# Kernel optimization log

Measured on AMD Instinct MI355X. Metric: run time of the kernel, lower is better.

## Reference

```python
import jax, jax.numpy as jnp
import numpy as np

DN = ('NCDHW', 'OIDHW', 'NCDHW')

def conv3d(x, w, b=None):
    y = jax.lax.conv_general_dilated(x, w, (1, 1, 1), 'SAME', dimension_numbers=DN)
    if b is not None:
        y = y + b[None, :, None, None, None]
    return y

def adaptive_conv(x, w):
    # x: [N,C,D,H,W], w: [N,27,D,H,W] (L1-normalized over channel dim)
    D, H, W = x.shape[2], x.shape[3], x.shape[4]
    p = jnp.pad(x, ((0, 0), (0, 0), (1, 1), (1, 1), (1, 1)))
    out = jnp.zeros_like(x)
    for i in range(3):
        for j in range(3):
            for k in range(3):
                t = i * 9 + j * 3 + k
                out = out + p[:, :, i:i + D, j:j + H, k:k + W] * w[:, t:t + 1]
    return out

def l1_normalize(w):
    # torch F.normalize(dim=1, p=1): denom clamped to 1e-12
    denom = jnp.maximum(jnp.sum(jnp.abs(w), axis=1, keepdims=True), 1e-12)
    return w / denom

def adaptive_block(x, w1, b1, w2, weights_src=None):
    src = x if weights_src is None else weights_src
    h = jax.nn.relu(conv3d(src, w1, b1))
    w = l1_normalize(conv3d(h, w2))  # [N,27,D,H,W]
    for _ in range(3):
        x = adaptive_conv(x, w)
    return x

def setup_inputs() -> dict:
    key = jax.random.key(0)
    ks = jax.random.split(key, 16)
    s = 0.05
    inp = {
        'x': jax.random.normal(ks[0], (1, 8, 128, 128, 128), dtype=jnp.float32),
        'ac1_w1': jax.random.normal(ks[1], (8, 8, 3, 3, 3), dtype=jnp.float32) * s,
        'ac1_b1': jnp.zeros((8,), dtype=jnp.float32),
        'ac1_w2': jax.random.normal(ks[2], (27, 8, 3, 3, 3), dtype=jnp.float32) * s,
        'ac2_w1': jax.random.normal(ks[3], (8, 8, 3, 3, 3), dtype=jnp.float32) * s,
        'ac2_b1': jnp.zeros((8,), dtype=jnp.float32),
        'ac2_w2': jax.random.normal(ks[4], (27, 8, 3, 3, 3), dtype=jnp.float32) * s,
        'ac3_w1': jax.random.normal(ks[5], (8, 8, 3, 3, 3), dtype=jnp.float32) * s,
        'ac3_b1': jnp.zeros((8,), dtype=jnp.float32),
        'ac3_w2': jax.random.normal(ks[6], (27, 8, 3, 3, 3), dtype=jnp.float32) * s,
        'mid_w': jax.random.normal(ks[7], (8, 8, 3, 3, 3), dtype=jnp.float32) * s,
        'mid_b': jnp.zeros((8,), dtype=jnp.float32),
        'out_w': jax.random.normal(ks[8], (1, 8, 3, 3, 3), dtype=jnp.float32) * s,
        'out_b': jnp.zeros((1,), dtype=jnp.float32),
    }
    return inp

def reference(x, ac1_w1, ac1_b1, ac1_w2, ac2_w1, ac2_b1, ac2_w2,
              ac3_w1, ac3_b1, ac3_w2, mid_w, mid_b, out_w, out_b):
    mid = adaptive_block(x, ac1_w1, ac1_b1, ac1_w2)
    mid = conv3d(mid, mid_w, mid_b)
    mid = adaptive_block(mid, ac2_w1, ac2_b1, ac2_w2)
    final = conv3d(mid, out_w, out_b)  # [N,1,D,H,W]
    final = adaptive_block(final, ac3_w1, ac3_b1, ac3_w2, weights_src=mid)
    return jnp.tanh(final)
```

## Files before the change

### kernel.cpp

```cpp
#include <hip/hip_runtime.h>
#include <math.h>

#define DSZ 128
#define VOX (DSZ*DSZ*DSZ)
#define PD  130

typedef _Float16 half8 __attribute__((ext_vector_type(8)));
typedef _Float16 half4 __attribute__((ext_vector_type(4)));
typedef _Float16 half2v __attribute__((ext_vector_type(2)));
typedef float float4v __attribute__((ext_vector_type(4)));


template<int CH>
__global__ __launch_bounds__(256) void zero_halo(_Float16* __restrict__ P)
{
    const int t = blockIdx.x * 256 + threadIdx.x;
    if (t >= PD * PD) return;
    const int zp = t / PD;
    const int yp = t - zp * PD;
    _Float16* row = P + (size_t)t * PD * CH;
    if (zp == 0 || zp == PD - 1 || yp == 0 || yp == PD - 1) {
        if (CH == 8) {
            half8 zz = {};
            for (int x = 0; x < PD; ++x) *(half8*)&row[x * 8] = zz;
        } else {
            for (int x = 0; x < PD; ++x) row[x] = (_Float16)0.0f;
        }
    } else {
        if (CH == 8) {
            half8 zz = {};
            *(half8*)&row[0] = zz;
            *(half8*)&row[(PD - 1) * 8] = zz;
        } else {
            row[0] = (_Float16)0.0f;
            row[PD - 1] = (_Float16)0.0f;
        }
    }
}

__global__ __launch_bounds__(256) void preformat(const float* __restrict__ w1a, const float* __restrict__ w1b,
                                                 const float* __restrict__ w1c, const float* __restrict__ outw,
                                                 const float* __restrict__ midw,
                                                 const float* __restrict__ w2a, const float* __restrict__ w2b,
                                                 const float* __restrict__ w2c, _Float16* __restrict__ WF)
{
    const int bid = blockIdx.x, tid = threadIdx.x;
    const float* src;
    _Float16* dst;
    int nelem, sz;
    if (bid < 3)       { src = bid == 0 ? w1a : bid == 1 ? w1b : w1c; dst = WF + bid * 3712; nelem = 8 * 216; sz = 16 * 29; }
    else if (bid == 3) { src = outw; dst = WF + 3 * 3712; nelem = 216;     sz = 16 * 29; }
    else if (bid == 4) { src = midw; dst = WF + 4 * 3712; nelem = 8 * 216; sz = 16 * 29; }
    else               { src = bid == 5 ? w2a : bid == 6 ? w2b : w2c; dst = WF + 5 * 3712 + (bid - 5) * 7424; nelem = 27 * 216; sz = 32 * 29; }
    for (int i = tid; i < sz; i += 256) ((half8*)dst)[i] = half8{};
    __syncthreads();
    for (int i = tid; i < nelem; i += 256) {
        const int oc = i / 216;
        const int rem = i - oc * 216;
        const int ic = rem / 27;
        const int tap = rem - ic * 27;
        dst[(oc * 29 + tap) * 8 + ic] = (_Float16)src[i];
    }
}

__global__ __launch_bounds__(256) void cast_hp(const float* __restrict__ in,
                                               _Float16* __restrict__ hp)
{
    const int idx = blockIdx.x * 256 + threadIdx.x;
    const int w = idx & 127;
    const int h = (idx >> 7) & 127;
    const int d = idx >> 14;
    half8 v;
    #pragma unroll
    for (int ic = 0; ic < 8; ++ic) v[ic] = (_Float16)in[(size_t)ic * VOX + idx];
    const int slot = ((d + 1) * PD + (h + 1)) * PD + (w + 1);
    *(half8*)&hp[(size_t)slot * 8] = v;
}

template<bool RELU>
__global__ __launch_bounds__(256) void conv8x8_mfma(const _Float16* __restrict__ DP,
                                                    const _Float16* __restrict__ WF,
                                                    const float* __restrict__ bias,
                                                    _Float16* __restrict__ HO)
{
    __shared__ _Float16 Wr[16 * 29 * 8];
    const int tid = threadIdx.x;
    for (int i = tid; i < 16 * 29; i += 256) ((half8*)Wr)[i] = ((const half8*)WF)[i];
    __syncthreads();

    const int b = ((blockIdx.x & 7) << 10) | (blockIdx.x >> 3);
    const int h0 = (b & 63) << 1;
    const int d  = b >> 6;
    const int lane = tid & 63;
    const int wv   = tid >> 6;
    const int col  = lane & 15;
    const int q    = lane >> 4;

    half8 af[7];
    #pragma unroll
    for (int c = 0; c < 7; ++c)
        af[c] = *(const half8*)&Wr[(col * 29 + (c * 4 + q)) * 8];

    const int base0 = ((d + 1) * PD + (h0 + 1)) * PD + 1 + wv * 32 + col;
    const _Float16* p[7];
    #pragma unroll
    for (int c = 0; c < 7; ++c) {
        const int tap = min(c * 4 + q, 26);
        const int dz = tap / 9, r9 = tap - dz * 9;
        const int dy = r9 / 3,  dx = r9 - dy * 3;
        p[c] = DP + (size_t)(base0 + ((dz - 1) * PD + (dy - 1)) * PD + (dx - 1)) * 8;
    }

    #pragma unroll
    for (int r = 0; r < 2; ++r) {
        #pragma unroll
        for (int t2 = 0; t2 < 2; ++t2) {
            float4v acc = {0.0f, 0.0f, 0.0f, 0.0f};
            #pragma unroll
            for (int c = 0; c < 7; ++c) {
                const half8 bv = *(const half8*)(p[c] + (r * PD + t2 * 16) * 8);
                acc = __builtin_amdgcn_mfma_f32_16x16x32_f16(af[c], bv, acc, 0, 0, 0);
            }
            if (q < 2) {
                const float4v bl = ((const float4v*)bias)[q];
                half4 hv;
                #pragma unroll
                for (int rr = 0; rr < 4; ++rr) {
                    float v = acc[rr] + bl[rr];
                    if (RELU) v = fmaxf(v, 0.0f);
                    hv[rr] = (_Float16)v;
                }
                *(half4*)&HO[(size_t)(base0 + r * PD + t2 * 16) * 8 + q * 4] = hv;
            }
        }
    }
}

__global__ __launch_bounds__(256) void conv8x1_mfma(const _Float16* __restrict__ DP,
                                                    const _Float16* __restrict__ WF,
                                                    const float* __restrict__ bias,
                                                    _Float16* __restrict__ F)
{
    __shared__ _Float16 Wr[16 * 29 * 8];
    const int tid = threadIdx.x;
    for (int i = tid; i < 16 * 29; i += 256) ((half8*)Wr)[i] = ((const half8*)WF)[i];
    __syncthreads();

    const int b = ((blockIdx.x & 7) << 10) | (blockIdx.x >> 3);
    const int h0 = (b & 63) << 1;
    const int d  = b >> 6;
    const int lane = tid & 63;
    const int wv   = tid >> 6;
    const int col  = lane & 15;
    const int q    = lane >> 4;

    half8 af[7];
    #pragma unroll
    for (int c = 0; c < 7; ++c)
        af[c] = *(const half8*)&Wr[(col * 29 + (c * 4 + q)) * 8];

    const int base0 = ((d + 1) * PD + (h0 + 1)) * PD + 1 + wv * 32 + col;
    const _Float16* p[7];
    #pragma unroll
    for (int c = 0; c < 7; ++c) {
        const int tap = min(c * 4 + q, 26);
        const int dz = tap / 9, r9 = tap - dz * 9;
        const int dy = r9 / 3,  dx = r9 - dy * 3;
        p[c] = DP + (size_t)(base0 + ((dz - 1) * PD + (dy - 1)) * PD + (dx - 1)) * 8;
    }

    const float b0 = bias[0];
    #pragma unroll
    for (int r = 0; r < 2; ++r) {
        #pragma unroll
        for (int t2 = 0; t2 < 2; ++t2) {
            float4v acc = {0.0f, 0.0f, 0.0f, 0.0f};
            #pragma unroll
            for (int c = 0; c < 7; ++c) {
                const half8 bv = *(const half8*)(p[c] + (r * PD + t2 * 16) * 8);
                acc = __builtin_amdgcn_mfma_f32_16x16x32_f16(af[c], bv, acc, 0, 0, 0);
            }
            if (q == 0)
                F[base0 + r * PD + t2 * 16] = (_Float16)(acc[0] + b0);
        }
    }
}

__global__ __launch_bounds__(256) void conv8x27n_mfma(const _Float16* __restrict__ HP,
                                                      const _Float16* __restrict__ WF,
                                                      _Float16* __restrict__ WB)
{
    __shared__ _Float16 Wr[32 * 29 * 8];
    const int tid = threadIdx.x;
    for (int i = tid; i < 32 * 29; i += 256) ((half8*)Wr)[i] = ((const half8*)WF)[i];
    __syncthreads();

    const int b = ((blockIdx.x & 7) << 10) | (blockIdx.x >> 3);
    const int h0 = (b & 63) << 1;
    const int d  = b >> 6;
    const int lane = tid & 63;
    const int wv   = tid >> 6;
    const int col  = lane & 15;
    const int q    = lane >> 4;

    half8 af[2][7];
    #pragma unroll
    for (int t = 0; t < 2; ++t)
        #pragma unroll
        for (int c = 0; c < 7; ++c)
            af[t][c] = *(const half8*)&Wr[((t * 16 + col) * 29 + (c * 4 + q)) * 8];

    const int base0 = ((d + 1) * PD + (h0 + 1)) * PD + 1 + wv * 32 + col;
    const _Float16* p[7];
    #pragma unroll
    for (int c = 0; c < 7; ++c) {
        const int tap = min(c * 4 + q, 26);
        const int dz = tap / 9, r9 = tap - dz * 9;
        const int dy = r9 / 3,  dx = r9 - dy * 3;
        p[c] = HP + (size_t)(base0 + ((dz - 1) * PD + (dy - 1)) * PD + (dx - 1)) * 8;
    }

    #pragma unroll
    for (int r = 0; r < 2; ++r) {
        #pragma unroll
        for (int t2 = 0; t2 < 2; ++t2) {
            float4v acc0 = {0.0f, 0.0f, 0.0f, 0.0f};
            float4v acc1 = {0.0f, 0.0f, 0.0f, 0.0f};
            #pragma unroll
            for (int c = 0; c < 7; ++c) {
                const half8 bv = *(const half8*)(p[c] + (r * PD + t2 * 16) * 8);
                acc0 = __builtin_amdgcn_mfma_f32_16x16x32_f16(af[0][c], bv, acc0, 0, 0, 0);
                acc1 = __builtin_amdgcn_mfma_f32_16x16x32_f16(af[1][c], bv, acc1, 0, 0, 0);
            }

            float s = 0.0f;
            #pragma unroll
            for (int rr = 0; rr < 4; ++rr) {
                s += fabsf(acc0[rr]);
                if (16 + q * 4 + rr < 27) s += fabsf(acc1[rr]);
            }
            s += __shfl_xor(s, 16);
            s += __shfl_xor(s, 32);
            const float rcp = 1.0f / fmaxf(s, 1e-12f);

            const int vox = (d << 14) + ((h0 + r) << 7) + wv * 32 + t2 * 16 + col;
            const size_t base = (size_t)vox * 32;
            half4 o0, o1;
            #pragma unroll
            for (int rr = 0; rr < 4; ++rr) {
                o0[rr] = (_Float16)(acc0[rr] * rcp);
                o1[rr] = (_Float16)(acc1[rr] * rcp);
            }
            *(half4*)&WB[base + q * 4]      = o0;
            *(half4*)&WB[base + 16 + q * 4] = o1;
        }
    }
}

__global__ __launch_bounds__(256) void aconv8i(const _Float16* __restrict__ in,
                                               const _Float16* __restrict__ wb,
                                               _Float16* __restrict__ out)
{
    const int b = ((blockIdx.x & 7) << 10) | (blockIdx.x >> 3);
    const int idx = b * 256 + threadIdx.x;
    const int w = idx & 127;
    const int h = (idx >> 7) & 127;
    const int d = idx >> 14;

    const size_t wbb = (size_t)idx * 32;
    const half8 wA = *(const half8*)(wb + wbb);
    const half8 wB = *(const half8*)(wb + wbb + 8);
    const half8 wC = *(const half8*)(wb + wbb + 16);
    const half8 wD = *(const half8*)(wb + wbb + 24);

    const int s0 = ((d + 1) * PD + (h + 1)) * PD + (w + 1);

    half2v a4[4];
    #pragma unroll
    for (int j = 0; j < 4; ++j) a4[j] = half2v{};

    #pragma unroll
    for (int dz = 0; dz < 3; dz++) {
        #pragma unroll
        for (int dy = 0; dy < 3; dy++) {
            const _Float16* rp = in + (size_t)(s0 + ((dz - 1) * PD + (dy - 1)) * PD) * 8;
            #pragma unroll
            for (int kw = 0; kw < 3; kw++) {
                const int tap = dz * 9 + dy * 3 + kw;
                const _Float16 wt = (tap < 8) ? wA[tap] : (tap < 16) ? wB[tap - 8]
                                 : (tap < 24) ? wC[tap - 16] : wD[tap - 24];
                half2v w2; w2[0] = wt; w2[1] = wt;
                const half8 hv = *(const half8*)(rp + (kw - 1) * 8);
                const half2v* h2 = (const half2v*)&hv;
                #pragma unroll
                for (int j = 0; j < 4; ++j)
                    a4[j] += h2[j] * w2;
            }
        }
    }

    half8 o;
    #pragma unroll
    for (int j = 0; j < 4; ++j) { o[2 * j] = a4[j][0]; o[2 * j + 1] = a4[j][1]; }
    *(half8*)&out[(size_t)s0 * 8] = o;
}

template<bool TANH>
__global__ __launch_bounds__(256) void aconv1h(const _Float16* __restrict__ in,
                                               const _Float16* __restrict__ wb,
                                               _Float16* __restrict__ outh,
                                               float* __restrict__ outf)
{
    const int b = ((blockIdx.x & 7) << 10) | (blockIdx.x >> 3);
    const int idx = b * 256 + threadIdx.x;
    const int w = idx & 127;
    const int h = (idx >> 7) & 127;
    const int d = idx >> 14;

    const size_t wbb = (size_t)idx * 32;
    const half8 wA = *(const half8*)(wb + wbb);
    const half8 wB = *(const half8*)(wb + wbb + 8);
    const half8 wC = *(const half8*)(wb + wbb + 16);
    const half8 wD = *(const half8*)(wb + wbb + 24);

    const int s0 = ((d + 1) * PD + (h + 1)) * PD + (w + 1);

    float acc = 0.0f;
    #pragma unroll
    for (int dz = 0; dz < 3; dz++) {
        #pragma unroll
        for (int dy = 0; dy < 3; dy++) {
            const _Float16* rp = in + s0 + ((dz - 1) * PD + (dy - 1)) * PD;
            #pragma unroll
            for (int kw = 0; kw < 3; kw++) {
                const int tap = dz * 9 + dy * 3 + kw;
                const _Float16 wt = (tap < 8) ? wA[tap] : (tap < 16) ? wB[tap - 8]
                                 : (tap < 24) ? wC[tap - 16] : wD[tap - 24];
                acc = fmaf((float)rp[kw - 1], (float)wt, acc);
            }
        }
    }

    if (TANH) outf[idx] = tanhf(acc);
    else      outh[s0] = (_Float16)acc;
}

extern "C" void kernel_launch(void* const* d_in, const int* in_sizes, int n_in,
                              void* d_out, int out_size, void* d_ws, size_t ws_size,
                              hipStream_t stream)
{
    const float* x      = (const float*)d_in[0];
    const float* ac1_w1 = (const float*)d_in[1];
    const float* ac1_b1 = (const float*)d_in[2];
    const float* ac1_w2 = (const float*)d_in[3];
    const float* ac2_w1 = (const float*)d_in[4];
    const float* ac2_b1 = (const float*)d_in[5];
    const float* ac2_w2 = (const float*)d_in[6];
    const float* ac3_w1 = (const float*)d_in[7];
    const float* ac3_b1 = (const float*)d_in[8];
    const float* ac3_w2 = (const float*)d_in[9];
    const float* mid_w  = (const float*)d_in[10];
    const float* mid_b  = (const float*)d_in[11];
    const float* out_w  = (const float*)d_in[12];
    const float* out_b  = (const float*)d_in[13];
    float* out = (float*)d_out;

    char* ws = (char*)d_ws;
    const size_t PS8 = (size_t)PD * PD * PD * 8 * 2;
    const size_t PS1 = (size_t)PD * PD * PD * 2;
    _Float16* P0 = (_Float16*)(ws);
    _Float16* P1 = (_Float16*)(ws + PS8);
    _Float16* WB = (_Float16*)(ws + 2 * PS8);
    _Float16* F1 = (_Float16*)(ws + 2 * PS8 + (size_t)134217728);
    _Float16* G1 = (_Float16*)(ws + 2 * PS8 + (size_t)134217728 + PS1);
    _Float16* F2 = (_Float16*)(ws + 2 * PS8 + (size_t)134217728 + 2 * PS1);
    _Float16* WF = (_Float16*)(ws + 2 * PS8 + (size_t)134217728 + 3 * PS1);
    _Float16* WF8_1  = WF;
    _Float16* WF8_2  = WF + 3712;
    _Float16* WF8_3  = WF + 7424;
    _Float16* WFo    = WF + 11136;
    _Float16* WFmid  = WF + 14848;
    _Float16* WF27_1 = WF + 18560;
    _Float16* WF27_2 = WF + 25984;
    _Float16* WF27_3 = WF + 33408;

    const dim3 blk(256);
    const dim3 gridT(VOX / 256);
    const dim3 gridM(VOX / 256);
    const dim3 gridZ((PD * PD + 255) / 256);

    zero_halo<8><<<gridZ, blk, 0, stream>>>(P0);
    zero_halo<8><<<gridZ, blk, 0, stream>>>(P1);
    zero_halo<1><<<gridZ, blk, 0, stream>>>(F1);
    zero_halo<1><<<gridZ, blk, 0, stream>>>(G1);
    zero_halo<1><<<gridZ, blk, 0, stream>>>(F2);
    preformat<<<dim3(8), blk, 0, stream>>>(ac1_w1, ac2_w1, ac3_w1, out_w, mid_w,
                                           ac1_w2, ac2_w2, ac3_w2, WF);

    cast_hp<<<gridT, blk, 0, stream>>>(x, P0);
    conv8x8_mfma<true ><<<gridM, blk, 0, stream>>>(P0, WF8_1, ac1_b1, P1);
    conv8x27n_mfma<<<gridM, blk, 0, stream>>>(P1, WF27_1, WB);
    aconv8i<<<gridT, blk, 0, stream>>>(P0, WB, P1);
    aconv8i<<<gridT, blk, 0, stream>>>(P1, WB, P0);
    aconv8i<<<gridT, blk, 0, stream>>>(P0, WB, P1);
    conv8x8_mfma<false><<<gridM, blk, 0, stream>>>(P1, WFmid, mid_b, P0);
    conv8x8_mfma<true ><<<gridM, blk, 0, stream>>>(P0, WF8_2, ac2_b1, P1);
    conv8x27n_mfma<<<gridM, blk, 0, stream>>>(P1, WF27_2, WB);
    aconv8i<<<gridT, blk, 0, stream>>>(P0, WB, P1);
    aconv8i<<<gridT, blk, 0, stream>>>(P1, WB, P0);
    aconv8i<<<gridT, blk, 0, stream>>>(P0, WB, P1);
    conv8x8_mfma<true ><<<gridM, blk, 0, stream>>>(P1, WF8_3, ac3_b1, P0);
    conv8x27n_mfma<<<gridM, blk, 0, stream>>>(P0, WF27_3, WB);
    conv8x1_mfma<<<gridM, blk, 0, stream>>>(P1, WFo, out_b, F1);
    aconv1h<false><<<gridT, blk, 0, stream>>>(F1, WB, G1, nullptr);
    aconv1h<false><<<gridT, blk, 0, stream>>>(G1, WB, F2, nullptr);
    aconv1h<true ><<<gridT, blk, 0, stream>>>(F2, WB, nullptr, out);
}
```

Before: 814.8 us.

## Fuse weight-generating conv with first adaptive conv pass using a third buffer

Adds a kernel that computes the 27-tap L1-normalized weights via MFMA and immediately applies the first adaptive convolution step in-register, writing both the weight buffer and the first output. This removes one aconv pass per block, including its re-read of the weight buffer and input. It needs an extra padded 8-channel buffer, so a fallback path keeps the old schedule when the workspace is too small. The fused kernel adds shuffle reductions and gathers, and it reorders the final-branch launches.

```diff
diff --git a/kernel.cpp b/kernel.cpp
--- a/kernel.cpp
+++ b/kernel.cpp
@@ -257,6 +257,139 @@
     }
 }
 
+template<int CH>
+__global__ __launch_bounds__(256) void conv8x27n_aconv(const _Float16* __restrict__ HP,
+                                                       const _Float16* __restrict__ WF,
+                                                       const _Float16* __restrict__ XP,
+                                                       _Float16* __restrict__ WB,
+                                                       _Float16* __restrict__ OUT)
+{
+    __shared__ _Float16 Wr[32 * 29 * 8];
+    const int tid = threadIdx.x;
+    for (int i = tid; i < 32 * 29; i += 256) ((half8*)Wr)[i] = ((const half8*)WF)[i];
+    __syncthreads();
+
+    const int b = ((blockIdx.x & 7) << 10) | (blockIdx.x >> 3);
+    const int h0 = (b & 63) << 1;
+    const int d  = b >> 6;
+    const int lane = tid & 63;
+    const int wv   = tid >> 6;
+    const int col  = lane & 15;
+    const int q    = lane >> 4;
+
+    half8 af[2][7];
+    #pragma unroll
+    for (int t = 0; t < 2; ++t)
+        #pragma unroll
+        for (int c = 0; c < 7; ++c)
+            af[t][c] = *(const half8*)&Wr[((t * 16 + col) * 29 + (c * 4 + q)) * 8];
+
+    const int base0 = ((d + 1) * PD + (h0 + 1)) * PD + 1 + wv * 32 + col;
+    const _Float16* p[7];
+    #pragma unroll
+    for (int c = 0; c < 7; ++c) {
+        const int tap = min(c * 4 + q, 26);
+        const int dz = tap / 9, r9 = tap - dz * 9;
+        const int dy = r9 / 3,  dx = r9 - dy * 3;
+        p[c] = HP + (size_t)(base0 + ((dz - 1) * PD + (dy - 1)) * PD + (dx - 1)) * 8;
+    }
+
+    int offlo[4], offhi[4];
+    #pragma unroll
+    for (int rr = 0; rr < 4; ++rr) {
+        { const int t = q * 4 + rr;
+          const int dz = t / 9, r9 = t - dz * 9, dy = r9 / 3, dx = r9 - dy * 3;
+          offlo[rr] = ((dz - 1) * PD + (dy - 1)) * PD + (dx - 1); }
+        { const int t = min(16 + q * 4 + rr, 26);
+          const int dz = t / 9, r9 = t - dz * 9, dy = r9 / 3, dx = r9 - dy * 3;
+          offhi[rr] = ((dz - 1) * PD + (dy - 1)) * PD + (dx - 1); }
+    }
+
+    #pragma unroll
+    for (int r = 0; r < 2; ++r) {
+        #pragma unroll
+        for (int t2 = 0; t2 < 2; ++t2) {
+            float4v acc0 = {0.0f, 0.0f, 0.0f, 0.0f};
+            float4v acc1 = {0.0f, 0.0f, 0.0f, 0.0f};
+            #pragma unroll
+            for (int c = 0; c < 7; ++c) {
+                const half8 bv = *(const half8*)(p[c] + (r * PD + t2 * 16) * 8);
+                acc0 = __builtin_amdgcn_mfma_f32_16x16x32_f16(af[0][c], bv, acc0, 0, 0, 0);
+                acc1 = __builtin_amdgcn_mfma_f32_16x16x32_f16(af[1][c], bv, acc1, 0, 0, 0);
+            }
+
+            float s = 0.0f;
+            #pragma unroll
+            for (int rr = 0; rr < 4; ++rr) {
+                s += fabsf(acc0[rr]);
+                if (16 + q * 4 + rr < 27) s += fabsf(acc1[rr]);
+            }
+            s += __shfl_xor(s, 16);
+            s += __shfl_xor(s, 32);
+            const float rcp = 1.0f / fmaxf(s, 1e-12f);
+
+            const int vox = (d << 14) + ((h0 + r) << 7) + wv * 32 + t2 * 16 + col;
+            const size_t base = (size_t)vox * 32;
+            half4 o0, o1;
+            #pragma unroll
+            for (int rr = 0; rr < 4; ++rr) {
+                o0[rr] = (_Float16)(acc0[rr] * rcp);
+                o1[rr] = (_Float16)(acc1[rr] * rcp);
+            }
+            *(half4*)&WB[base + q * 4]      = o0;
+            *(half4*)&WB[base + 16 + q * 4] = o1;
+
+            const int sslot = base0 + r * PD + t2 * 16;
+            if (CH == 8) {
+                half2v a4[4];
+                #pragma unroll
+                for (int j = 0; j < 4; ++j) a4[j] = half2v{};
+                #pragma unroll
+                for (int rr = 0; rr < 4; ++rr) {
+                    const _Float16 wl = o0[rr];
+                    const half8 xl = *(const half8*)&XP[(size_t)(sslot + offlo[rr]) * 8];
+                    half2v w2l; w2l[0] = wl; w2l[1] = wl;
+                    const half2v* xl2 = (const half2v*)&xl;
+                    #pragma unroll
+                    for (int j = 0; j < 4; ++j) a4[j] += xl2[j] * w2l;
+
+                    const _Float16 wh = o1[rr];
+                    const half8 xh = *(const half8*)&XP[(size_t)(sslot + offhi[rr]) * 8];
+                    half2v w2h; w2h[0] = wh; w2h[1] = wh;
+                    const half2v* xh2 = (const half2v*)&xh;
+                    #pragma unroll
+                    for (int j = 0; j < 4; ++j) a4[j] += xh2[j] * w2h;
+                }
+                #pragma unroll
+                for (int j = 0; j < 4; ++j) {
+                    int v = *(int*)&a4[j];
+                    int u = __shfl_xor(v, 16);
+                    a4[j] += *(half2v*)&u;
+                    int v2 = *(int*)&a4[j];
+                    int u2 = __shfl_xor(v2, 32);
+                    a4[j] += *(half2v*)&u2;
+                }
+                if (q == 0) {
+                    half8 o;
+                    #pragma unroll
+                    for (int j = 0; j < 4; ++j) { o[2 * j] = a4[j][0]; o[2 * j + 1] = a4[j][1]; }
+                    *(half8*)&OUT[(size_t)sslot * 8] = o;
+                }
+            } else {
+                float acc = 0.0f;
+                #pragma unroll
+                for (int rr = 0; rr < 4; ++rr) {
+                    acc = fmaf((float)XP[sslot + offlo[rr]], (float)o0[rr], acc);
+                    acc = fmaf((float)XP[sslot + offhi[rr]], (float)o1[rr], acc);
+                }
+                acc += __shfl_xor(acc, 16);
+                acc += __shfl_xor(acc, 32);
+                if (q == 0) OUT[sslot] = (_Float16)acc;
+            }
+        }
+    }
+}
+
 __global__ __launch_bounds__(256) void aconv8i(const _Float16* __restrict__ in,
                                                const _Float16* __restrict__ wb,
                                                _Float16* __restrict__ out)
@@ -368,51 +501,99 @@
     char* ws = (char*)d_ws;
     const size_t PS8 = (size_t)PD * PD * PD * 8 * 2;
     const size_t PS1 = (size_t)PD * PD * PD * 2;
-    _Float16* P0 = (_Float16*)(ws);
-    _Float16* P1 = (_Float16*)(ws + PS8);
-    _Float16* WB = (_Float16*)(ws + 2 * PS8);
-    _Float16* F1 = (_Float16*)(ws + 2 * PS8 + (size_t)134217728);
-    _Float16* G1 = (_Float16*)(ws + 2 * PS8 + (size_t)134217728 + PS1);
-    _Float16* F2 = (_Float16*)(ws + 2 * PS8 + (size_t)134217728 + 2 * PS1);
-    _Float16* WF = (_Float16*)(ws + 2 * PS8 + (size_t)134217728 + 3 * PS1);
-    _Float16* WF8_1  = WF;
-    _Float16* WF8_2  = WF + 3712;
-    _Float16* WF8_3  = WF + 7424;
-    _Float16* WFo    = WF + 11136;
-    _Float16* WFmid  = WF + 14848;
-    _Float16* WF27_1 = WF + 18560;
-    _Float16* WF27_2 = WF + 25984;
-    _Float16* WF27_3 = WF + 33408;
+    const size_t WBsz = (size_t)134217728;
+    const size_t WFsz = (size_t)81920;
+    const size_t need_fused = 3 * PS8 + WBsz + 3 * PS1 + WFsz;
 
     const dim3 blk(256);
     const dim3 gridT(VOX / 256);
     const dim3 gridM(VOX / 256);
     const dim3 gridZ((PD * PD + 255) / 256);
 
-    zero_halo<8><<<gridZ, blk, 0, stream>>>(P0);
-    zero_halo<8><<<gridZ, blk, 0, stream>>>(P1);
-    zero_halo<1><<<gridZ, blk, 0, stream>>>(F1);
-    zero_halo<1><<<gridZ, blk, 0, stream>>>(G1);
-    zero_halo<1><<<gridZ, blk, 0, stream>>>(F2);
-    preformat<<<dim3(8), blk, 0, stream>>>(ac1_w1, ac2_w1, ac3_w1, out_w, mid_w,
-                                           ac1_w2, ac2_w2, ac3_w2, WF);
-
-    cast_hp<<<gridT, blk, 0, stream>>>(x, P0);
-    conv8x8_mfma<true ><<<gridM, blk, 0, stream>>>(P0, WF8_1, ac1_b1, P1);
-    conv8x27n_mfma<<<gridM, blk, 0, stream>>>(P1, WF27_1, WB);
-    aconv8i<<<gridT, blk, 0, stream>>>(P0, WB, P1);
-    aconv8i<<<gridT, blk, 0, stream>>>(P1, WB, P0);
-    aconv8i<<<gridT, blk, 0, stream>>>(P0, WB, P1);
-    conv8x8_mfma<false><<<gridM, blk, 0, stream>>>(P1, WFmid, mid_b, P0);
-    conv8x8_mfma<true ><<<gridM, blk, 0, stream>>>(P0, WF8_2, ac2_b1, P1);
-    conv8x27n_mfma<<<gridM, blk, 0, stream>>>(P1, WF27_2, WB);
-    aconv8i<<<gridT, blk, 0, stream>>>(P0, WB, P1);
-    aconv8i<<<gridT, blk, 0, stream>>>(P1, WB, P0);
-    aconv8i<<<gridT, blk, 0, stream>>>(P0, WB, P1);
-    conv8x8_mfma<true ><<<gridM, blk, 0, stream>>>(P1, WF8_3, ac3_b1, P0);
-    conv8x27n_mfma<<<gridM, blk, 0, stream>>>(P0, WF27_3, WB);
-    conv8x1_mfma<<<gridM, blk, 0, stream>>>(P1, WFo, out_b, F1);
-    aconv1h<false><<<gridT, blk, 0, stream>>>(F1, WB, G1, nullptr);
-    aconv1h<false><<<gridT, blk, 0, stream>>>(G1, WB, F2, nullptr);
-    aconv1h<true ><<<gridT, blk, 0, stream>>>(F2, WB, nullptr, out);
-}
+    if (ws_size >= need_fused) {
+        _Float16* P0 = (_Float16*)(ws);
+        _Float16* P1 = (_Float16*)(ws + PS8);
+        _Float16* P2 = (_Float16*)(ws + 2 * PS8);
+        _Float16* WB = (_Float16*)(ws + 3 * PS8);
+        _Float16* F1 = (_Float16*)(ws + 3 * PS8 + WBsz);
+        _Float16* G1 = (_Float16*)(ws + 3 * PS8 + WBsz + PS1);
+        _Float16* F2 = (_Float16*)(ws + 3 * PS8 + WBsz + 2 * PS1);
+        _Float16* WF = (_Float16*)(ws + 3 * PS8 + WBsz + 3 * PS1);
+        _Float16* WF8_1  = WF;
+        _Float16* WF8_2  = WF + 3712;
+        _Float16* WF8_3  = WF + 7424;
+        _Float16* WFo    = WF + 11136;
+        _Float16* WFmid  = WF + 14848;
+        _Float16* WF27_1 = WF + 18560;
+        _Float16* WF27_2 = WF + 25984;
+        _Float16* WF27_3 = WF + 33408;
+
+        zero_halo<8><<<gridZ, blk, 0, stream>>>(P0);
+        zero_halo<8><<<gridZ, blk, 0, stream>>>(P1);
+        zero_halo<8><<<gridZ, blk, 0, stream>>>(P2);
+        zero_halo<1><<<gridZ, blk, 0, stream>>>(F1);
+        zero_halo<1><<<gridZ, blk, 0, stream>>>(G1);
+        zero_halo<1><<<gridZ, blk, 0, stream>>>(F2);
+        preformat<<<dim3(8), blk, 0, stream>>>(ac1_w1, ac2_w1, ac3_w1, out_w, mid_w,
+                                               ac1_w2, ac2_w2, ac3_w2, WF);
+
+        cast_hp<<<gridT, blk, 0, stream>>>(x, P0);
+        conv8x8_mfma<true ><<<gridM, blk, 0, stream>>>(P0, WF8_1, ac1_b1, P1);
+        conv8x27n_aconv<8><<<gridM, blk, 0, stream>>>(P1, WF27_1, P0, WB, P2);
+        aconv8i<<<gridT, blk, 0, stream>>>(P2, WB, P0);
+        aconv8i<<<gridT, blk, 0, stream>>>(P0, WB, P1);
+        conv8x8_mfma<false><<<gridM, blk, 0, stream>>>(P1, WFmid, mid_b, P0);
+        conv8x8_mfma<true ><<<gridM, blk, 0, stream>>>(P0, WF8_2, ac2_b1, P1);
+        conv8x27n_aconv<8><<<gridM, blk, 0, stream>>>(P1, WF27_2, P0, WB, P2);
+        aconv8i<<<gridT, blk, 0, stream>>>(P2, WB, P0);
+        aconv8i<<<gridT, blk, 0, stream>>>(P0, WB, P1);
+        conv8x1_mfma<<<gridM, blk, 0, stream>>>(P1, WFo, out_b, F1);
+        conv8x8_mfma<true ><<<gridM, blk, 0, stream>>>(P1, WF8_3, ac3_b1, P0);
+        conv8x27n_aconv<1><<<gridM, blk, 0, stream>>>(P0, WF27_3, F1, WB, G1);
+        aconv1h<false><<<gridT, blk, 0, stream>>>(G1, WB, F2, nullptr);
+        aconv1h<true ><<<gridT, blk, 0, stream>>>(F2, WB, nullptr, out);
+    } else {
+        _Float16* P0 = (_Float16*)(ws);
+        _Float16* P1 = (_Float16*)(ws + PS8);
+        _Float16* WB = (_Float16*)(ws + 2 * PS8);
+        _Float16* F1 = (_Float16*)(ws + 2 * PS8 + WBsz);
+        _Float16* G1 = (_Float16*)(ws + 2 * PS8 + WBsz + PS1);
+        _Float16* F2 = (_Float16*)(ws + 2 * PS8 + WBsz + 2 * PS1);
+        _Float16* WF = (_Float16*)(ws + 2 * PS8 + WBsz + 3 * PS1);
+        _Float16* WF8_1  = WF;
+        _Float16* WF8_2  = WF + 3712;
+        _Float16* WF8_3  = WF + 7424;
+        _Float16* WFo    = WF + 11136;
+        _Float16* WFmid  = WF + 14848;
+        _Float16* WF27_1 = WF + 18560;
+        _Float16* WF27_2 = WF + 25984;
+        _Float16* WF27_3 = WF + 33408;
+
+        zero_halo<8><<<gridZ, blk, 0, stream>>>(P0);
+        zero_halo<8><<<gridZ, blk, 0, stream>>>(P1);
+        zero_halo<1><<<gridZ, blk, 0, stream>>>(F1);
+        zero_halo<1><<<gridZ, blk, 0, stream>>>(G1);
+        zero_halo<1><<<gridZ, blk, 0, stream>>>(F2);
+        preformat<<<dim3(8), blk, 0, stream>>>(ac1_w1, ac2_w1, ac3_w1, out_w, mid_w,
+                                               ac1_w2, ac2_w2, ac3_w2, WF);
+
+        cast_hp<<<gridT, blk, 0, stream>>>(x, P0);
+        conv8x8_mfma<true ><<<gridM, blk, 0, stream>>>(P0, WF8_1, ac1_b1, P1);
+        conv8x27n_mfma<<<gridM, blk, 0, stream>>>(P1, WF27_1, WB);
+        aconv8i<<<gridT, blk, 0, stream>>>(P0, WB, P1);
+        aconv8i<<<gridT, blk, 0, stream>>>(P1, WB, P0);
+        aconv8i<<<gridT, blk, 0, stream>>>(P0, WB, P1);
+        conv8x8_mfma<false><<<gridM, blk, 0, stream>>>(P1, WFmid, mid_b, P0);
+        conv8x8_mfma<true ><<<gridM, blk, 0, stream>>>(P0, WF8_2, ac2_b1, P1);
+        conv8x27n_mfma<<<gridM, blk, 0, stream>>>(P1, WF27_2, WB);
+        aconv8i<<<gridT, blk, 0, stream>>>(P0, WB, P1);
+        aconv8i<<<gridT, blk, 0, stream>>>(P1, WB, P0);
+        aconv8i<<<gridT, blk, 0, stream>>>(P0, WB, P1);
+        conv8x8_mfma<true ><<<gridM, blk, 0, stream>>>(P1, WF8_3, ac3_b1, P0);
+        conv8x27n_mfma<<<gridM, blk, 0, stream>>>(P0, WF27_3, WB);
+        conv8x1_mfma<<<gridM, blk, 0, stream>>>(P1, WFo, out_b, F1);
+        aconv1h<false><<<gridT, blk, 0, stream>>>(F1, WB, G1, nullptr);
+        aconv1h<false><<<gridT, blk, 0, stream>>>(G1, WB, F2, nullptr);
+        aconv1h<true ><<<gridT, blk, 0, stream>>>(F2, WB, nullptr, out);
+    }
+}
```

New measurement: 887.4 us. +8.9%, slower.
